# Kernel optimization log

Hardware: AMD Instinct MI355X
Metric: run time of the kernel (lower is better)

The kernel has to match this reference:

```python
import jax, jax.numpy as jnp
import numpy as np

MARGIN = 1.0  # init kwarg; squared=True so no sqrt/eps path


def setup_inputs() -> dict:
    key = jax.random.key(0)
    k1, k2 = jax.random.split(key)
    N, D, C = 512, 512, 64
    embeddings = jax.random.normal(k1, (N, D), dtype=jnp.float32)
    labels = jax.random.randint(k2, (N,), 0, C, dtype=jnp.int64)
    return {"embeddings": embeddings, "labels": labels}


def reference(embeddings, labels):
    N = embeddings.shape[0]
    # Pairwise squared Euclidean distances D[i, j] = ||e_i - e_j||^2 (gram form;
    # mathematically identical to the per-triplet gather of squared differences).
    sq = jnp.sum(embeddings * embeddings, axis=1)  # [N]
    dist = sq[:, None] + sq[None, :] - 2.0 * (embeddings @ embeddings.T)  # [N, N]

    # Valid-pair masks: pos = same label, different index; neg = different label.
    same_label = labels[:, None] == labels[None, :]
    diff_index = ~jnp.eye(N, dtype=bool)
    pos_mask = diff_index & same_label  # [a, p]
    neg_mask = diff_index & ~same_label  # [a, n]

    # Triplet mask [a, p, n]; instead of nonzero + gather, mask the dense
    # d_ap - d_an + margin tensor and do an online masked mean.
    triplet_mask = pos_mask[:, :, None] & neg_mask[:, None, :]
    terms = jax.nn.relu(dist[:, :, None] - dist[:, None, :] + MARGIN)  # [N, N, N]
    masked = jnp.where(triplet_mask, terms, jnp.float32(0.0))
    count = jnp.maximum(jnp.sum(triplet_mask), 1).astype(embeddings.dtype)
    loss = jnp.sum(masked) / count  # mean over all valid triplets (batch-all)
    return loss
```

## Files before the change

kernel.cpp:

```cpp
#include <hip/hip_runtime.h>
#include <hip/hip_bf16.h>

#define NN 512
#define DD 512
#define MARGIN_F 1.0f

constexpr int BM = 64, BN = 64, BK = 32, KSPLIT = 4, KCH = DD / KSPLIT;

__global__ __launch_bounds__(256) void k_gram(const float* __restrict__ E,
                                              float* __restrict__ part,
                                              float* __restrict__ diag) {
    __shared__ float As[BK][BM + 4];
    __shared__ float Bs[BK][BN + 4];
    const int tid = threadIdx.x;
    const int tx = tid & 15, ty = tid >> 4;
    const int row0 = blockIdx.y * BM, col0 = blockIdx.x * BN;
    const int z = blockIdx.z;
    const int k0 = z * KCH;
    float acc[4][4] = {};
    for (int kt = 0; kt < KCH; kt += BK) {
#pragma unroll
        for (int q = 0; q < 2; ++q) {
            int idx = tid + q * 256;
            int r = idx >> 3;
            int kv = idx & 7;
            float4 va = *reinterpret_cast<const float4*>(
                &E[(size_t)(row0 + r) * DD + k0 + kt + kv * 4]);
            As[kv * 4 + 0][r] = va.x;
            As[kv * 4 + 1][r] = va.y;
            As[kv * 4 + 2][r] = va.z;
            As[kv * 4 + 3][r] = va.w;
            float4 vb = *reinterpret_cast<const float4*>(
                &E[(size_t)(col0 + r) * DD + k0 + kt + kv * 4]);
            Bs[kv * 4 + 0][r] = vb.x;
            Bs[kv * 4 + 1][r] = vb.y;
            Bs[kv * 4 + 2][r] = vb.z;
            Bs[kv * 4 + 3][r] = vb.w;
        }
        __syncthreads();
#pragma unroll
        for (int k = 0; k < BK; ++k) {
            float4 av = *reinterpret_cast<const float4*>(&As[k][ty * 4]);
            float4 bv = *reinterpret_cast<const float4*>(&Bs[k][tx * 4]);
            float a[4] = {av.x, av.y, av.z, av.w};
            float b[4] = {bv.x, bv.y, bv.z, bv.w};
#pragma unroll
            for (int i = 0; i < 4; ++i)
#pragma unroll
                for (int j = 0; j < 4; ++j) acc[i][j] += a[i] * b[j];
        }
        __syncthreads();
    }
    float* pz = part + (size_t)z * NN * NN;
#pragma unroll
    for (int i = 0; i < 4; ++i) {
        int gi = row0 + ty * 4 + i;
        float4 st = make_float4(acc[i][0], acc[i][1], acc[i][2], acc[i][3]);
        *reinterpret_cast<float4*>(&pz[(size_t)gi * NN + col0 + tx * 4]) = st;
    }
    if (row0 == col0 && tx == ty) {
#pragma unroll
        for (int i = 0; i < 4; ++i) diag[z * NN + row0 + ty * 4 + i] = acc[i][i];
    }
}

__global__ __launch_bounds__(256) void k_triplet(const float* __restrict__ part,
                                                 const float* __restrict__ diag,
                                                 const int* __restrict__ labels,
                                                 float* __restrict__ s_part,
                                                 int* __restrict__ np_part) {
    const int a = blockIdx.x;
    const int tid = threadIdx.x;
    __shared__ float posv[NN];
    __shared__ int nPos;
    if (tid == 0) nPos = 0;
    __syncthreads();
    const int la = labels[a];
    const float g_aa = diag[0 * NN + a] + diag[1 * NN + a] + diag[2 * NN + a] + diag[3 * NN + a];
    float dval[2];
    int neg[2];
#pragma unroll
    for (int q = 0; q < 2; ++q) {
        int j = tid + q * 256;
        float g_aj = part[(size_t)0 * NN * NN + (size_t)a * NN + j] +
                     part[(size_t)1 * NN * NN + (size_t)a * NN + j] +
                     part[(size_t)2 * NN * NN + (size_t)a * NN + j] +
                     part[(size_t)3 * NN * NN + (size_t)a * NN + j];
        float g_jj = diag[0 * NN + j] + diag[1 * NN + j] + diag[2 * NN + j] + diag[3 * NN + j];
        float d = g_aa + g_jj - 2.0f * g_aj;
        dval[q] = d;
        neg[q] = 0;
        if (j != a) {
            if (labels[j] == la) {
                int p = atomicAdd(&nPos, 1);
                posv[p] = d;
            } else {
                neg[q] = 1;
            }
        }
    }
    __syncthreads();
    const int np = nPos;
    float acc = 0.f;
#pragma unroll
    for (int q = 0; q < 2; ++q) {
        if (neg[q]) {
            float d = dval[q] - MARGIN_F;
            for (int p = 0; p < np; ++p) acc += fmaxf(posv[p] - d, 0.f);
        }
    }
#pragma unroll
    for (int off = 32; off > 0; off >>= 1) acc += __shfl_down(acc, off);
    __shared__ float wsum[4];
    if ((tid & 63) == 0) wsum[tid >> 6] = acc;
    __syncthreads();
    if (tid == 0) {
        s_part[a] = wsum[0] + wsum[1] + wsum[2] + wsum[3];
        np_part[a] = np;
    }
}

__global__ __launch_bounds__(256) void k_reduce(const float* __restrict__ s_part,
                                                const int* __restrict__ np_part,
                                                float* __restrict__ out) {
    const int tid = threadIdx.x;
    double s = 0.0;
    long long c = 0;
    for (int i = tid; i < NN; i += 256) {
        s += (double)s_part[i];
        int np = np_part[i];
        c += (long long)np * (511 - np);
    }
#pragma unroll
    for (int off = 32; off > 0; off >>= 1) {
        s += __shfl_down(s, off);
        c += __shfl_down(c, off);
    }
    __shared__ double ws_[4];
    __shared__ long long wc_[4];
    if ((tid & 63) == 0) {
        ws_[tid >> 6] = s;
        wc_[tid >> 6] = c;
    }
    __syncthreads();
    if (tid == 0) {
        double tot = ws_[0] + ws_[1] + ws_[2] + ws_[3];
        long long cnt = wc_[0] + wc_[1] + wc_[2] + wc_[3];
        if (cnt < 1) cnt = 1;
        out[0] = (float)(tot / (double)cnt);
    }
}

extern "C" void kernel_launch(void* const* d_in, const int* in_sizes, int n_in,
                              void* d_out, int out_size, void* d_ws, size_t ws_size,
                              hipStream_t stream) {
    const float* E = (const float*)d_in[0];
    const int* labels = (const int*)d_in[1];
    float* out = (float*)d_out;

    float* part = (float*)d_ws;
    float* diag = (float*)((char*)d_ws + (size_t)KSPLIT * NN * NN * 4);
    float* s_part = (float*)((char*)diag + (size_t)KSPLIT * NN * 4);
    int* np_part = (int*)((char*)s_part + (size_t)NN * 4);

    k_gram<<<dim3(NN / BN, NN / BM, KSPLIT), 256, 0, stream>>>(E, part, diag);
    k_triplet<<<NN, 256, 0, stream>>>(part, diag, labels, s_part, np_part);
    k_reduce<<<1, 256, 0, stream>>>(s_part, np_part, out);
}
```

Before: 69.49 us.

## Fuse gram, triplet and reduce kernels into one cooperative kernel with grid syncs

Replaces the three separate launches with a single cooperative kernel of 256 blocks. Each block first computes one gram tile and K-split, then after a grid sync handles two anchors of the triplet loss, and after a second grid sync block 0 does the final reduction. The shared As buffer is reused to hold the positive distances. This removes two kernel launches and the gaps between them, at the cost of grid-wide barriers and only 256 blocks in the triplet phase, half as many as before.

Measured after the change: 173.1 us. 149% more time.

```diff
diff --git a/kernel.cpp b/kernel.cpp
--- a/kernel.cpp
+++ b/kernel.cpp
@@ -1,5 +1,8 @@
 #include <hip/hip_runtime.h>
 #include <hip/hip_bf16.h>
+#include <hip/hip_cooperative_groups.h>
+
+namespace cg = cooperative_groups;
 
 #define NN 512
 #define DD 512
@@ -7,147 +10,159 @@
 
 constexpr int BM = 64, BN = 64, BK = 32, KSPLIT = 4, KCH = DD / KSPLIT;
 
-__global__ __launch_bounds__(256) void k_gram(const float* __restrict__ E,
-                                              float* __restrict__ part,
-                                              float* __restrict__ diag) {
+__global__ __launch_bounds__(256) void k_fused(const float* __restrict__ E,
+                                               const int* __restrict__ labels,
+                                               float* __restrict__ part,
+                                               float* __restrict__ diag,
+                                               float* __restrict__ s_part,
+                                               int* __restrict__ np_part,
+                                               float* __restrict__ out) {
+    cg::grid_group grid = cg::this_grid();
+
     __shared__ float As[BK][BM + 4];
     __shared__ float Bs[BK][BN + 4];
+    __shared__ int nPosSh;
+    __shared__ float wsum[4];
+    __shared__ double ws_[4];
+    __shared__ long long wc_[4];
+    float* posv = &As[0][0];
+
     const int tid = threadIdx.x;
-    const int tx = tid & 15, ty = tid >> 4;
-    const int row0 = blockIdx.y * BM, col0 = blockIdx.x * BN;
-    const int z = blockIdx.z;
-    const int k0 = z * KCH;
-    float acc[4][4] = {};
-    for (int kt = 0; kt < KCH; kt += BK) {
+    const int bid = blockIdx.x;
+
+    {
+        const int tileId = bid & 63;
+        const int z = bid >> 6;
+        const int row0 = (tileId >> 3) * BM;
+        const int col0 = (tileId & 7) * BN;
+        const int k0 = z * KCH;
+        const int tx = tid & 15, ty = tid >> 4;
+        float acc[4][4] = {};
+        for (int kt = 0; kt < KCH; kt += BK) {
+#pragma unroll
+            for (int q = 0; q < 2; ++q) {
+                int idx = tid + q * 256;
+                int r = idx >> 3;
+                int kv = idx & 7;
+                float4 va = *reinterpret_cast<const float4*>(
+                    &E[(size_t)(row0 + r) * DD + k0 + kt + kv * 4]);
+                As[kv * 4 + 0][r] = va.x;
+                As[kv * 4 + 1][r] = va.y;
+                As[kv * 4 + 2][r] = va.z;
+                As[kv * 4 + 3][r] = va.w;
+                float4 vb = *reinterpret_cast<const float4*>(
+                    &E[(size_t)(col0 + r) * DD + k0 + kt + kv * 4]);
+                Bs[kv * 4 + 0][r] = vb.x;
+                Bs[kv * 4 + 1][r] = vb.y;
+                Bs[kv * 4 + 2][r] = vb.z;
+                Bs[kv * 4 + 3][r] = vb.w;
+            }
+            __syncthreads();
+#pragma unroll
+            for (int k = 0; k < BK; ++k) {
+                float4 av = *reinterpret_cast<const float4*>(&As[k][ty * 4]);
+                float4 bv = *reinterpret_cast<const float4*>(&Bs[k][tx * 4]);
+                float a[4] = {av.x, av.y, av.z, av.w};
+                float b[4] = {bv.x, bv.y, bv.z, bv.w};
+#pragma unroll
+                for (int i = 0; i < 4; ++i)
+#pragma unroll
+                    for (int j = 0; j < 4; ++j) acc[i][j] += a[i] * b[j];
+            }
+            __syncthreads();
+        }
+        float* pz = part + (size_t)z * NN * NN;
+#pragma unroll
+        for (int i = 0; i < 4; ++i) {
+            int gi = row0 + ty * 4 + i;
+            float4 st = make_float4(acc[i][0], acc[i][1], acc[i][2], acc[i][3]);
+            *reinterpret_cast<float4*>(&pz[(size_t)gi * NN + col0 + tx * 4]) = st;
+        }
+        if (row0 == col0 && tx == ty) {
+#pragma unroll
+            for (int i = 0; i < 4; ++i) diag[z * NN + row0 + ty * 4 + i] = acc[i][i];
+        }
+    }
+
+    __threadfence();
+    grid.sync();
+
+    for (int s = 0; s < 2; ++s) {
+        const int a = (bid << 1) + s;
+        if (tid == 0) nPosSh = 0;
+        __syncthreads();
+        const int la = labels[a];
+        const float g_aa =
+            diag[a] + diag[NN + a] + diag[2 * NN + a] + diag[3 * NN + a];
+        float dval[2];
+        int neg[2];
 #pragma unroll
         for (int q = 0; q < 2; ++q) {
-            int idx = tid + q * 256;
-            int r = idx >> 3;
-            int kv = idx & 7;
-            float4 va = *reinterpret_cast<const float4*>(
-                &E[(size_t)(row0 + r) * DD + k0 + kt + kv * 4]);
-            As[kv * 4 + 0][r] = va.x;
-            As[kv * 4 + 1][r] = va.y;
-            As[kv * 4 + 2][r] = va.z;
-            As[kv * 4 + 3][r] = va.w;
-            float4 vb = *reinterpret_cast<const float4*>(
-                &E[(size_t)(col0 + r) * DD + k0 + kt + kv * 4]);
-            Bs[kv * 4 + 0][r] = vb.x;
-            Bs[kv * 4 + 1][r] = vb.y;
-            Bs[kv * 4 + 2][r] = vb.z;
-            Bs[kv * 4 + 3][r] = vb.w;
+            int j = tid + q * 256;
+            float g_aj = part[(size_t)0 * NN * NN + (size_t)a * NN + j] +
+                         part[(size_t)1 * NN * NN + (size_t)a * NN + j] +
+                         part[(size_t)2 * NN * NN + (size_t)a * NN + j] +
+                         part[(size_t)3 * NN * NN + (size_t)a * NN + j];
+            float g_jj = diag[j] + diag[NN + j] + diag[2 * NN + j] + diag[3 * NN + j];
+            float d = g_aa + g_jj - 2.0f * g_aj;
+            dval[q] = d;
+            neg[q] = 0;
+            if (j != a) {
+                if (labels[j] == la) {
+                    int p = atomicAdd(&nPosSh, 1);
+                    posv[p] = d;
+                } else {
+                    neg[q] = 1;
+                }
+            }
         }
         __syncthreads();
+        const int np = nPosSh;
+        float acc = 0.f;
 #pragma unroll
-        for (int k = 0; k < BK; ++k) {
-            float4 av = *reinterpret_cast<const float4*>(&As[k][ty * 4]);
-            float4 bv = *reinterpret_cast<const float4*>(&Bs[k][tx * 4]);
-            float a[4] = {av.x, av.y, av.z, av.w};
-            float b[4] = {bv.x, bv.y, bv.z, bv.w};
+        for (int q = 0; q < 2; ++q) {
+            if (neg[q]) {
+                float d = dval[q] - MARGIN_F;
+                for (int p = 0; p < np; ++p) acc += fmaxf(posv[p] - d, 0.f);
+            }
+        }
 #pragma unroll
-            for (int i = 0; i < 4; ++i)
+        for (int off = 32; off > 0; off >>= 1) acc += __shfl_down(acc, off);
+        if ((tid & 63) == 0) wsum[tid >> 6] = acc;
+        __syncthreads();
+        if (tid == 0) {
+            s_part[a] = wsum[0] + wsum[1] + wsum[2] + wsum[3];
+            np_part[a] = np;
+        }
+    }
+
+    __threadfence();
+    grid.sync();
+
+    if (bid == 0) {
+        double sd = 0.0;
+        long long c = 0;
+        for (int i = tid; i < NN; i += 256) {
+            sd += (double)s_part[i];
+            int np = np_part[i];
+            c += (long long)np * (511 - np);
+        }
 #pragma unroll
-                for (int j = 0; j < 4; ++j) acc[i][j] += a[i] * b[j];
+        for (int off = 32; off > 0; off >>= 1) {
+            sd += __shfl_down(sd, off);
+            c += __shfl_down(c, off);
+        }
+        if ((tid & 63) == 0) {
+            ws_[tid >> 6] = sd;
+            wc_[tid >> 6] = c;
         }
         __syncthreads();
-    }
-    float* pz = part + (size_t)z * NN * NN;
-#pragma unroll
-    for (int i = 0; i < 4; ++i) {
-        int gi = row0 + ty * 4 + i;
-        float4 st = make_float4(acc[i][0], acc[i][1], acc[i][2], acc[i][3]);
-        *reinterpret_cast<float4*>(&pz[(size_t)gi * NN + col0 + tx * 4]) = st;
-    }
-    if (row0 == col0 && tx == ty) {
-#pragma unroll
-        for (int i = 0; i < 4; ++i) diag[z * NN + row0 + ty * 4 + i] = acc[i][i];
-    }
-}
-
-__global__ __launch_bounds__(256) void k_triplet(const float* __restrict__ part,
-                                                 const float* __restrict__ diag,
-                                                 const int* __restrict__ labels,
-                                                 float* __restrict__ s_part,
-                                                 int* __restrict__ np_part) {
-    const int a = blockIdx.x;
-    const int tid = threadIdx.x;
-    __shared__ float posv[NN];
-    __shared__ int nPos;
-    if (tid == 0) nPos = 0;
-    __syncthreads();
-    const int la = labels[a];
-    const float g_aa = diag[0 * NN + a] + diag[1 * NN + a] + diag[2 * NN + a] + diag[3 * NN + a];
-    float dval[2];
-    int neg[2];
-#pragma unroll
-    for (int q = 0; q < 2; ++q) {
-        int j = tid + q * 256;
-        float g_aj = part[(size_t)0 * NN * NN + (size_t)a * NN + j] +
-                     part[(size_t)1 * NN * NN + (size_t)a * NN + j] +
-                     part[(size_t)2 * NN * NN + (size_t)a * NN + j] +
-                     part[(size_t)3 * NN * NN + (size_t)a * NN + j];
-        float g_jj = diag[0 * NN + j] + diag[1 * NN + j] + diag[2 * NN + j] + diag[3 * NN + j];
-        float d = g_aa + g_jj - 2.0f * g_aj;
-        dval[q] = d;
-        neg[q] = 0;
-        if (j != a) {
-            if (labels[j] == la) {
-                int p = atomicAdd(&nPos, 1);
-                posv[p] = d;
-            } else {
-                neg[q] = 1;
-            }
+        if (tid == 0) {
+            double tot = ws_[0] + ws_[1] + ws_[2] + ws_[3];
+            long long cnt = wc_[0] + wc_[1] + wc_[2] + wc_[3];
+            if (cnt < 1) cnt = 1;
+            out[0] = (float)(tot / (double)cnt);
         }
-    }
-    __syncthreads();
-    const int np = nPos;
-    float acc = 0.f;
-#pragma unroll
-    for (int q = 0; q < 2; ++q) {
-        if (neg[q]) {
-            float d = dval[q] - MARGIN_F;
-            for (int p = 0; p < np; ++p) acc += fmaxf(posv[p] - d, 0.f);
-        }
-    }
-#pragma unroll
-    for (int off = 32; off > 0; off >>= 1) acc += __shfl_down(acc, off);
-    __shared__ float wsum[4];
-    if ((tid & 63) == 0) wsum[tid >> 6] = acc;
-    __syncthreads();
-    if (tid == 0) {
-        s_part[a] = wsum[0] + wsum[1] + wsum[2] + wsum[3];
-        np_part[a] = np;
-    }
-}
-
-__global__ __launch_bounds__(256) void k_reduce(const float* __restrict__ s_part,
-                                                const int* __restrict__ np_part,
-                                                float* __restrict__ out) {
-    const int tid = threadIdx.x;
-    double s = 0.0;
-    long long c = 0;
-    for (int i = tid; i < NN; i += 256) {
-        s += (double)s_part[i];
-        int np = np_part[i];
-        c += (long long)np * (511 - np);
-    }
-#pragma unroll
-    for (int off = 32; off > 0; off >>= 1) {
-        s += __shfl_down(s, off);
-        c += __shfl_down(c, off);
-    }
-    __shared__ double ws_[4];
-    __shared__ long long wc_[4];
-    if ((tid & 63) == 0) {
-        ws_[tid >> 6] = s;
-        wc_[tid >> 6] = c;
-    }
-    __syncthreads();
-    if (tid == 0) {
-        double tot = ws_[0] + ws_[1] + ws_[2] + ws_[3];
-        long long cnt = wc_[0] + wc_[1] + wc_[2] + wc_[3];
-        if (cnt < 1) cnt = 1;
-        out[0] = (float)(tot / (double)cnt);
     }
 }
 
@@ -163,7 +178,9 @@
     float* s_part = (float*)((char*)diag + (size_t)KSPLIT * NN * 4);
     int* np_part = (int*)((char*)s_part + (size_t)NN * 4);
 
-    k_gram<<<dim3(NN / BN, NN / BM, KSPLIT), 256, 0, stream>>>(E, part, diag);
-    k_triplet<<<NN, 256, 0, stream>>>(part, diag, labels, s_part, np_part);
-    k_reduce<<<1, 256, 0, stream>>>(s_part, np_part, out);
+    void* args[] = {(void*)&E,      (void*)&labels,  (void*)&part,
+                    (void*)&diag,   (void*)&s_part,  (void*)&np_part,
+                    (void*)&out};
+    hipLaunchCooperativeKernel((void*)k_fused, dim3(256), dim3(256), args, 0,
+                               stream);
 }
```

## Fuse distance computation and triplet accumulation into one kernel per anchor pair

Applied to the files above, without the earlier changes.

Replaces the split-K gram GEMM plus triplet kernel with a single fused kernel. Each block handles two anchors and computes the squared differences directly against all 512 embeddings, streaming them through a swizzled shared-memory tile with register prefetch. This removes the 4MB partial-gram write and read-back and one kernel launch. In exchange every block re-reads the whole embedding matrix (256 blocks × 1MB, mostly from L2), does direct-difference arithmetic instead of a tiled GEMM, and caps posv at 64 positives per anchor.

Result: slower. 142.2 us (+104.6%).

```diff
diff --git a/kernel.cpp b/kernel.cpp
--- a/kernel.cpp
+++ b/kernel.cpp
@@ -4,133 +4,115 @@
 #define NN 512
 #define DD 512
 #define MARGIN_F 1.0f
+#define KT 64
+#define NKT (DD / KT)
 
-constexpr int BM = 64, BN = 64, BK = 32, KSPLIT = 4, KCH = DD / KSPLIT;
+__global__ __launch_bounds__(256) void k_fused(const float* __restrict__ E,
+                                               const int* __restrict__ labels,
+                                               float* __restrict__ s_part,
+                                               int* __restrict__ c_part) {
+    __shared__ float tile[256][KT];
+    __shared__ float ea[2][DD];
+    __shared__ int lab[NN];
+    __shared__ float posv[2][64];
+    __shared__ int nP[2];
+    __shared__ float wsum[4];
 
-__global__ __launch_bounds__(256) void k_gram(const float* __restrict__ E,
-                                              float* __restrict__ part,
-                                              float* __restrict__ diag) {
-    __shared__ float As[BK][BM + 4];
-    __shared__ float Bs[BK][BN + 4];
     const int tid = threadIdx.x;
-    const int tx = tid & 15, ty = tid >> 4;
-    const int row0 = blockIdx.y * BM, col0 = blockIdx.x * BN;
-    const int z = blockIdx.z;
-    const int k0 = z * KCH;
-    float acc[4][4] = {};
-    for (int kt = 0; kt < KCH; kt += BK) {
+    const int bid = blockIdx.x;
+    const int a0 = bid * 2, a1 = a0 + 1;
+
+    if (tid == 0) { nP[0] = 0; nP[1] = 0; }
+    {
+        int row = tid >> 7, c4 = (tid & 127) * 4;
+        *(float4*)&ea[row][c4] = *(const float4*)&E[(size_t)(a0 + row) * DD + c4];
+        lab[tid] = labels[tid];
+        lab[tid + 256] = labels[tid + 256];
+    }
+
+    float4 ld[16];
+    float dacc[2][2] = {{0.f, 0.f}, {0.f, 0.f}};
+
+    auto issue = [&](int jbase, int kt) {
 #pragma unroll
-        for (int q = 0; q < 2; ++q) {
-            int idx = tid + q * 256;
-            int r = idx >> 3;
-            int kv = idx & 7;
-            float4 va = *reinterpret_cast<const float4*>(
-                &E[(size_t)(row0 + r) * DD + k0 + kt + kv * 4]);
-            As[kv * 4 + 0][r] = va.x;
-            As[kv * 4 + 1][r] = va.y;
-            As[kv * 4 + 2][r] = va.z;
-            As[kv * 4 + 3][r] = va.w;
-            float4 vb = *reinterpret_cast<const float4*>(
-                &E[(size_t)(col0 + r) * DD + k0 + kt + kv * 4]);
-            Bs[kv * 4 + 0][r] = vb.x;
-            Bs[kv * 4 + 1][r] = vb.y;
-            Bs[kv * 4 + 2][r] = vb.z;
-            Bs[kv * 4 + 3][r] = vb.w;
+        for (int p = 0; p < 16; ++p) {
+            int idx = p * 256 + tid;
+            int r = idx >> 4, kv = idx & 15;
+            ld[p] = *(const float4*)&E[(size_t)(jbase + r) * DD + kt * KT + kv * 4];
         }
-        __syncthreads();
+    };
+    auto swrite = [&]() {
 #pragma unroll
-        for (int k = 0; k < BK; ++k) {
-            float4 av = *reinterpret_cast<const float4*>(&As[k][ty * 4]);
-            float4 bv = *reinterpret_cast<const float4*>(&Bs[k][tx * 4]);
-            float a[4] = {av.x, av.y, av.z, av.w};
-            float b[4] = {bv.x, bv.y, bv.z, bv.w};
+        for (int p = 0; p < 16; ++p) {
+            int idx = p * 256 + tid;
+            int r = idx >> 4, kv = idx & 15;
+            *(float4*)&tile[r][(kv ^ (r & 7)) << 2] = ld[p];
+        }
+    };
+
+    issue(0, 0);
+
 #pragma unroll
-            for (int i = 0; i < 4; ++i)
+    for (int jt = 0; jt < 2; ++jt) {
+#pragma unroll 1
+        for (int kt = 0; kt < NKT; ++kt) {
+            __syncthreads();
+            swrite();
+            __syncthreads();
+            if (jt == 0) {
+                if (kt < NKT - 1) issue(0, kt + 1);
+                else issue(256, 0);
+            } else {
+                if (kt < NKT - 1) issue(256, kt + 1);
+            }
 #pragma unroll
-                for (int j = 0; j < 4; ++j) acc[i][j] += a[i] * b[j];
+            for (int c = 0; c < 16; ++c) {
+                float4 v = *(const float4*)&tile[tid][(c ^ (tid & 7)) << 2];
+                float4 w0 = *(const float4*)&ea[0][kt * KT + (c << 2)];
+                float4 w1 = *(const float4*)&ea[1][kt * KT + (c << 2)];
+                float t;
+                t = w0.x - v.x; dacc[jt][0] += t * t;
+                t = w0.y - v.y; dacc[jt][0] += t * t;
+                t = w0.z - v.z; dacc[jt][0] += t * t;
+                t = w0.w - v.w; dacc[jt][0] += t * t;
+                t = w1.x - v.x; dacc[jt][1] += t * t;
+                t = w1.y - v.y; dacc[jt][1] += t * t;
+                t = w1.z - v.z; dacc[jt][1] += t * t;
+                t = w1.w - v.w; dacc[jt][1] += t * t;
+            }
         }
-        __syncthreads();
     }
-    float* pz = part + (size_t)z * NN * NN;
+
+    const int la0 = lab[a0], la1 = lab[a1];
+    const int j0 = tid, j1 = tid + 256;
+    if (j0 != a0 && lab[j0] == la0) { int p = atomicAdd(&nP[0], 1); posv[0][p] = dacc[0][0]; }
+    if (j0 != a1 && lab[j0] == la1) { int p = atomicAdd(&nP[1], 1); posv[1][p] = dacc[0][1]; }
+    if (j1 != a0 && lab[j1] == la0) { int p = atomicAdd(&nP[0], 1); posv[0][p] = dacc[1][0]; }
+    if (j1 != a1 && lab[j1] == la1) { int p = atomicAdd(&nP[1], 1); posv[1][p] = dacc[1][1]; }
+    __syncthreads();
+    const int np0 = nP[0], np1 = nP[1];
+    float acc = 0.f;
+    if (lab[j0] != la0) { float b = MARGIN_F - dacc[0][0]; for (int p = 0; p < np0; ++p) acc += fmaxf(posv[0][p] + b, 0.f); }
+    if (lab[j0] != la1) { float b = MARGIN_F - dacc[0][1]; for (int p = 0; p < np1; ++p) acc += fmaxf(posv[1][p] + b, 0.f); }
+    if (lab[j1] != la0) { float b = MARGIN_F - dacc[1][0]; for (int p = 0; p < np0; ++p) acc += fmaxf(posv[0][p] + b, 0.f); }
+    if (lab[j1] != la1) { float b = MARGIN_F - dacc[1][1]; for (int p = 0; p < np1; ++p) acc += fmaxf(posv[1][p] + b, 0.f); }
+
 #pragma unroll
-    for (int i = 0; i < 4; ++i) {
-        int gi = row0 + ty * 4 + i;
-        float4 st = make_float4(acc[i][0], acc[i][1], acc[i][2], acc[i][3]);
-        *reinterpret_cast<float4*>(&pz[(size_t)gi * NN + col0 + tx * 4]) = st;
-    }
-    if (row0 == col0 && tx == ty) {
-#pragma unroll
-        for (int i = 0; i < 4; ++i) diag[z * NN + row0 + ty * 4 + i] = acc[i][i];
+    for (int off = 32; off > 0; off >>= 1) acc += __shfl_down(acc, off);
+    if ((tid & 63) == 0) wsum[tid >> 6] = acc;
+    __syncthreads();
+    if (tid == 0) {
+        s_part[bid] = wsum[0] + wsum[1] + wsum[2] + wsum[3];
+        c_part[bid] = np0 * (511 - np0) + np1 * (511 - np1);
     }
 }
 
-__global__ __launch_bounds__(256) void k_triplet(const float* __restrict__ part,
-                                                 const float* __restrict__ diag,
-                                                 const int* __restrict__ labels,
-                                                 float* __restrict__ s_part,
-                                                 int* __restrict__ np_part) {
-    const int a = blockIdx.x;
+__global__ __launch_bounds__(256) void k_finalize(const float* __restrict__ s_part,
+                                                  const int* __restrict__ c_part,
+                                                  float* __restrict__ out) {
     const int tid = threadIdx.x;
-    __shared__ float posv[NN];
-    __shared__ int nPos;
-    if (tid == 0) nPos = 0;
-    __syncthreads();
-    const int la = labels[a];
-    const float g_aa = diag[0 * NN + a] + diag[1 * NN + a] + diag[2 * NN + a] + diag[3 * NN + a];
-    float dval[2];
-    int neg[2];
-#pragma unroll
-    for (int q = 0; q < 2; ++q) {
-        int j = tid + q * 256;
-        float g_aj = part[(size_t)0 * NN * NN + (size_t)a * NN + j] +
-                     part[(size_t)1 * NN * NN + (size_t)a * NN + j] +
-                     part[(size_t)2 * NN * NN + (size_t)a * NN + j] +
-                     part[(size_t)3 * NN * NN + (size_t)a * NN + j];
-        float g_jj = diag[0 * NN + j] + diag[1 * NN + j] + diag[2 * NN + j] + diag[3 * NN + j];
-        float d = g_aa + g_jj - 2.0f * g_aj;
-        dval[q] = d;
-        neg[q] = 0;
-        if (j != a) {
-            if (labels[j] == la) {
-                int p = atomicAdd(&nPos, 1);
-                posv[p] = d;
-            } else {
-                neg[q] = 1;
-            }
-        }
-    }
-    __syncthreads();
-    const int np = nPos;
-    float acc = 0.f;
-#pragma unroll
-    for (int q = 0; q < 2; ++q) {
-        if (neg[q]) {
-            float d = dval[q] - MARGIN_F;
-            for (int p = 0; p < np; ++p) acc += fmaxf(posv[p] - d, 0.f);
-        }
-    }
-#pragma unroll
-    for (int off = 32; off > 0; off >>= 1) acc += __shfl_down(acc, off);
-    __shared__ float wsum[4];
-    if ((tid & 63) == 0) wsum[tid >> 6] = acc;
-    __syncthreads();
-    if (tid == 0) {
-        s_part[a] = wsum[0] + wsum[1] + wsum[2] + wsum[3];
-        np_part[a] = np;
-    }
-}
-
-__global__ __launch_bounds__(256) void k_reduce(const float* __restrict__ s_part,
-                                                const int* __restrict__ np_part,
-                                                float* __restrict__ out) {
-    const int tid = threadIdx.x;
-    double s = 0.0;
-    long long c = 0;
-    for (int i = tid; i < NN; i += 256) {
-        s += (double)s_part[i];
-        int np = np_part[i];
-        c += (long long)np * (511 - np);
-    }
+    double s = (double)s_part[tid];
+    long long c = (long long)c_part[tid];
 #pragma unroll
     for (int off = 32; off > 0; off >>= 1) {
         s += __shfl_down(s, off);
@@ -138,10 +120,7 @@
     }
     __shared__ double ws_[4];
     __shared__ long long wc_[4];
-    if ((tid & 63) == 0) {
-        ws_[tid >> 6] = s;
-        wc_[tid >> 6] = c;
-    }
+    if ((tid & 63) == 0) { ws_[tid >> 6] = s; wc_[tid >> 6] = c; }
     __syncthreads();
     if (tid == 0) {
         double tot = ws_[0] + ws_[1] + ws_[2] + ws_[3];
@@ -158,12 +137,9 @@
     const int* labels = (const int*)d_in[1];
     float* out = (float*)d_out;
 
-    float* part = (float*)d_ws;
-    float* diag = (float*)((char*)d_ws + (size_t)KSPLIT * NN * NN * 4);
-    float* s_part = (float*)((char*)diag + (size_t)KSPLIT * NN * 4);
-    int* np_part = (int*)((char*)s_part + (size_t)NN * 4);
+    float* s_part = (float*)d_ws;
+    int* c_part = (int*)((char*)d_ws + 2048);
 
-    k_gram<<<dim3(NN / BN, NN / BM, KSPLIT), 256, 0, stream>>>(E, part, diag);
-    k_triplet<<<NN, 256, 0, stream>>>(part, diag, labels, s_part, np_part);
-    k_reduce<<<1, 256, 0, stream>>>(s_part, np_part, out);
+    k_fused<<<256, 256, 0, stream>>>(E, labels, s_part, c_part);
+    k_finalize<<<1, 256, 0, stream>>>(s_part, c_part, out);
 }
```

## Fuse norms and distance epilogue into a single full-K gram kernel

Applied to the files above, without the earlier changes.

Replaces the split-K gram kernel, which wrote four partial Gram matrices plus diagonals, with a 32x32-tile kernel. It runs over the full K dimension with register-prefetched loads, computes squared row norms on the fly and writes the final distance matrix directly. The triplet kernel then reads one distance value per pair instead of summing four partials and diagonals, and the positive-distance buffer shrinks to 64 entries. This is meant to remove partial-matrix traffic and redundant reductions. The trade-offs are a smaller 2x2 per-thread tile with lower arithmetic intensity, and an assumption that no class has more than 64 members.

Measured after the change: 74.28 us. 6.9% more time.

```diff
diff --git a/kernel.cpp b/kernel.cpp
--- a/kernel.cpp
+++ b/kernel.cpp
@@ -4,90 +4,108 @@
 #define NN 512
 #define DD 512
 #define MARGIN_F 1.0f
+#define BKD 64
+#define NSTEP (DD / BKD)
 
-constexpr int BM = 64, BN = 64, BK = 32, KSPLIT = 4, KCH = DD / KSPLIT;
+__global__ __launch_bounds__(256) void k_dist(const float* __restrict__ E,
+                                              float* __restrict__ dist) {
+    __shared__ float As[BKD][34];
+    __shared__ float Bs[BKD][34];
+    __shared__ float sqA[32], sqB[32];
 
-__global__ __launch_bounds__(256) void k_gram(const float* __restrict__ E,
-                                              float* __restrict__ part,
-                                              float* __restrict__ diag) {
-    __shared__ float As[BK][BM + 4];
-    __shared__ float Bs[BK][BN + 4];
     const int tid = threadIdx.x;
-    const int tx = tid & 15, ty = tid >> 4;
-    const int row0 = blockIdx.y * BM, col0 = blockIdx.x * BN;
-    const int z = blockIdx.z;
-    const int k0 = z * KCH;
-    float acc[4][4] = {};
-    for (int kt = 0; kt < KCH; kt += BK) {
+    const int R = blockIdx.y * 32, C = blockIdx.x * 32;
+    const int r0 = tid >> 4;
+    const int kv = tid & 15;
+
+    float4 pa0, pa1, pb0, pb1;
+    auto issue = [&](int kt) {
+        const float* pA = E + (size_t)(R + r0) * DD + kt * BKD + kv * 4;
+        pa0 = *(const float4*)pA;
+        pa1 = *(const float4*)(pA + 16 * DD);
+        const float* pB = E + (size_t)(C + r0) * DD + kt * BKD + kv * 4;
+        pb0 = *(const float4*)pB;
+        pb1 = *(const float4*)(pB + 16 * DD);
+    };
+
+    float sa0 = 0.f, sa1 = 0.f, sb0 = 0.f, sb1 = 0.f;
+    float a00 = 0.f, a01 = 0.f, a10 = 0.f, a11 = 0.f;
+
+    issue(0);
+#pragma unroll 1
+    for (int kt = 0; kt < NSTEP; ++kt) {
+        sa0 += pa0.x * pa0.x + pa0.y * pa0.y + pa0.z * pa0.z + pa0.w * pa0.w;
+        sa1 += pa1.x * pa1.x + pa1.y * pa1.y + pa1.z * pa1.z + pa1.w * pa1.w;
+        sb0 += pb0.x * pb0.x + pb0.y * pb0.y + pb0.z * pb0.z + pb0.w * pb0.w;
+        sb1 += pb1.x * pb1.x + pb1.y * pb1.y + pb1.z * pb1.z + pb1.w * pb1.w;
+        __syncthreads();
+        {
+            const float fa0[4] = {pa0.x, pa0.y, pa0.z, pa0.w};
+            const float fa1[4] = {pa1.x, pa1.y, pa1.z, pa1.w};
+            const float fb0[4] = {pb0.x, pb0.y, pb0.z, pb0.w};
+            const float fb1[4] = {pb1.x, pb1.y, pb1.z, pb1.w};
 #pragma unroll
-        for (int q = 0; q < 2; ++q) {
-            int idx = tid + q * 256;
-            int r = idx >> 3;
-            int kv = idx & 7;
-            float4 va = *reinterpret_cast<const float4*>(
-                &E[(size_t)(row0 + r) * DD + k0 + kt + kv * 4]);
-            As[kv * 4 + 0][r] = va.x;
-            As[kv * 4 + 1][r] = va.y;
-            As[kv * 4 + 2][r] = va.z;
-            As[kv * 4 + 3][r] = va.w;
-            float4 vb = *reinterpret_cast<const float4*>(
-                &E[(size_t)(col0 + r) * DD + k0 + kt + kv * 4]);
-            Bs[kv * 4 + 0][r] = vb.x;
-            Bs[kv * 4 + 1][r] = vb.y;
-            Bs[kv * 4 + 2][r] = vb.z;
-            Bs[kv * 4 + 3][r] = vb.w;
+            for (int c = 0; c < 4; ++c) {
+                As[kv * 4 + c][r0] = fa0[c];
+                As[kv * 4 + c][r0 + 16] = fa1[c];
+                Bs[kv * 4 + c][r0] = fb0[c];
+                Bs[kv * 4 + c][r0 + 16] = fb1[c];
+            }
         }
         __syncthreads();
+        if (kt < NSTEP - 1) issue(kt + 1);
 #pragma unroll
-        for (int k = 0; k < BK; ++k) {
-            float4 av = *reinterpret_cast<const float4*>(&As[k][ty * 4]);
-            float4 bv = *reinterpret_cast<const float4*>(&Bs[k][tx * 4]);
-            float a[4] = {av.x, av.y, av.z, av.w};
-            float b[4] = {bv.x, bv.y, bv.z, bv.w};
+        for (int k = 0; k < BKD; ++k) {
+            float2 av = *(const float2*)&As[k][r0 * 2];
+            float2 bv = *(const float2*)&Bs[k][kv * 2];
+            a00 += av.x * bv.x;
+            a01 += av.x * bv.y;
+            a10 += av.y * bv.x;
+            a11 += av.y * bv.y;
+        }
+    }
+
 #pragma unroll
-            for (int i = 0; i < 4; ++i)
-#pragma unroll
-                for (int j = 0; j < 4; ++j) acc[i][j] += a[i] * b[j];
-        }
-        __syncthreads();
+    for (int m = 1; m <= 8; m <<= 1) {
+        sa0 += __shfl_xor(sa0, m);
+        sa1 += __shfl_xor(sa1, m);
+        sb0 += __shfl_xor(sb0, m);
+        sb1 += __shfl_xor(sb1, m);
     }
-    float* pz = part + (size_t)z * NN * NN;
-#pragma unroll
-    for (int i = 0; i < 4; ++i) {
-        int gi = row0 + ty * 4 + i;
-        float4 st = make_float4(acc[i][0], acc[i][1], acc[i][2], acc[i][3]);
-        *reinterpret_cast<float4*>(&pz[(size_t)gi * NN + col0 + tx * 4]) = st;
+    if (kv == 0) {
+        sqA[r0] = sa0;
+        sqA[r0 + 16] = sa1;
+        sqB[r0] = sb0;
+        sqB[r0 + 16] = sb1;
     }
-    if (row0 == col0 && tx == ty) {
-#pragma unroll
-        for (int i = 0; i < 4; ++i) diag[z * NN + row0 + ty * 4 + i] = acc[i][i];
-    }
+    __syncthreads();
+
+    const float qa0 = sqA[r0 * 2], qa1 = sqA[r0 * 2 + 1];
+    const float qb0 = sqB[kv * 2], qb1 = sqB[kv * 2 + 1];
+    float2 o0 = make_float2(qa0 + qb0 - 2.f * a00, qa0 + qb1 - 2.f * a01);
+    float2 o1 = make_float2(qa1 + qb0 - 2.f * a10, qa1 + qb1 - 2.f * a11);
+    *(float2*)&dist[(size_t)(R + r0 * 2) * NN + C + kv * 2] = o0;
+    *(float2*)&dist[(size_t)(R + r0 * 2 + 1) * NN + C + kv * 2] = o1;
 }
 
-__global__ __launch_bounds__(256) void k_triplet(const float* __restrict__ part,
-                                                 const float* __restrict__ diag,
+__global__ __launch_bounds__(256) void k_triplet(const float* __restrict__ dist,
                                                  const int* __restrict__ labels,
                                                  float* __restrict__ s_part,
                                                  int* __restrict__ np_part) {
     const int a = blockIdx.x;
     const int tid = threadIdx.x;
-    __shared__ float posv[NN];
+    __shared__ float posv[64];
     __shared__ int nPos;
+    __shared__ float wsum[4];
     if (tid == 0) nPos = 0;
     __syncthreads();
     const int la = labels[a];
-    const float g_aa = diag[0 * NN + a] + diag[1 * NN + a] + diag[2 * NN + a] + diag[3 * NN + a];
     float dval[2];
     int neg[2];
 #pragma unroll
     for (int q = 0; q < 2; ++q) {
         int j = tid + q * 256;
-        float g_aj = part[(size_t)0 * NN * NN + (size_t)a * NN + j] +
-                     part[(size_t)1 * NN * NN + (size_t)a * NN + j] +
-                     part[(size_t)2 * NN * NN + (size_t)a * NN + j] +
-                     part[(size_t)3 * NN * NN + (size_t)a * NN + j];
-        float g_jj = diag[0 * NN + j] + diag[1 * NN + j] + diag[2 * NN + j] + diag[3 * NN + j];
-        float d = g_aa + g_jj - 2.0f * g_aj;
+        float d = dist[(size_t)a * NN + j];
         dval[q] = d;
         neg[q] = 0;
         if (j != a) {
@@ -105,13 +123,12 @@
 #pragma unroll
     for (int q = 0; q < 2; ++q) {
         if (neg[q]) {
-            float d = dval[q] - MARGIN_F;
-            for (int p = 0; p < np; ++p) acc += fmaxf(posv[p] - d, 0.f);
+            float b = MARGIN_F - dval[q];
+            for (int p = 0; p < np; ++p) acc += fmaxf(posv[p] + b, 0.f);
         }
     }
 #pragma unroll
     for (int off = 32; off > 0; off >>= 1) acc += __shfl_down(acc, off);
-    __shared__ float wsum[4];
     if ((tid & 63) == 0) wsum[tid >> 6] = acc;
     __syncthreads();
     if (tid == 0) {
@@ -158,12 +175,11 @@
     const int* labels = (const int*)d_in[1];
     float* out = (float*)d_out;
 
-    float* part = (float*)d_ws;
-    float* diag = (float*)((char*)d_ws + (size_t)KSPLIT * NN * NN * 4);
-    float* s_part = (float*)((char*)diag + (size_t)KSPLIT * NN * 4);
+    float* dist = (float*)d_ws;
+    float* s_part = (float*)((char*)d_ws + (size_t)NN * NN * 4);
     int* np_part = (int*)((char*)s_part + (size_t)NN * 4);
 
-    k_gram<<<dim3(NN / BN, NN / BM, KSPLIT), 256, 0, stream>>>(E, part, diag);
-    k_triplet<<<NN, 256, 0, stream>>>(part, diag, labels, s_part, np_part);
+    k_dist<<<dim3(16, 16), 256, 0, stream>>>(E, dist);
+    k_triplet<<<NN, 256, 0, stream>>>(dist, labels, s_part, np_part);
     k_reduce<<<1, 256, 0, stream>>>(s_part, np_part, out);
 }
```
